# Optimization experiments

Measured on AMD Instinct MI355X. Metric: run time of the kernel, lower is better.

## Reference

```python
import jax, jax.numpy as jnp
import numpy as np

B, S, D_MODEL, H_DIM = 8, 4096, 512, 120  # h = 1, so d_k = h_dim = 120
NEG_INF = jnp.float32(-1e9)
L2_EPS = 1e-12  # F.normalize eps


def setup_inputs() -> dict:
    key = jax.random.key(0)
    k_q, k_m, k_w, k_wt = jax.random.split(key, 4)
    query = jax.random.normal(k_q, (B, S, D_MODEL), dtype=jnp.float32)
    mask = jax.random.randint(k_m, (B, S, S), 0, 2, dtype=jnp.int32)
    # q_linear params (kaiming-uniform-ish init scale)
    lim = 1.0 / np.sqrt(D_MODEL)
    w_q = jax.random.uniform(k_w, (H_DIM, D_MODEL), jnp.float32, -lim, lim)
    b_q = jnp.zeros((H_DIM,), jnp.float32)
    # weight_tensor: shape (h, d_k) = (1, 120), xavier-uniform scale
    wt_lim = np.sqrt(6.0 / (1 + H_DIM))
    weight_tensor = jax.random.uniform(k_wt, (1, H_DIM), jnp.float32, -wt_lim, wt_lim)
    return {"query": query, "mask": mask, "w_q": w_q, "b_q": b_q,
            "weight_tensor": weight_tensor}


def reference(query, mask, w_q, b_q, weight_tensor):
    # context = q_linear(query).view(B, -1, h_dim); with h=1 the view is identity
    context = jnp.einsum("bsd,kd->bsk", query, w_q) + b_q          # [B, S, 120]
    # weighted then L2-normalized (cosine-similarity) features
    ctx = context * weight_tensor[:, None, :]                        # bcast (1,1,120)
    norm = jnp.sqrt(jnp.sum(ctx * ctx, axis=-1, keepdims=True))
    ctx_n = ctx / jnp.maximum(norm, L2_EPS)
    scores = jnp.einsum("bqk,bpk->bqp", ctx_n, ctx_n)               # [B, S, S]
    scores = jnp.where(mask == 0, NEG_INF, scores)                   # masked_fill
    return jax.nn.softmax(scores, axis=-1)                           # dropout: eval/identity
```

## Files before the change

### kernel.cpp

```cpp
#include <hip/hip_runtime.h>
#include <hip/hip_bf16.h>
#include <stdint.h>

#define BATCH 8
#define SEQ   4096
#define DM    512
#define HD    120

typedef __bf16   v8bf  __attribute__((ext_vector_type(8)));
typedef float    v4f   __attribute__((ext_vector_type(4)));
typedef int      i4    __attribute__((ext_vector_type(4)));
typedef uint32_t u32x2 __attribute__((ext_vector_type(2)));
typedef uint32_t u32x4 __attribute__((ext_vector_type(4)));
typedef float    f32x4 __attribute__((ext_vector_type(4)));

static __device__ __forceinline__ ushort f2bf(float x) {
  uint32_t u = __builtin_bit_cast(uint32_t, x);
  return (ushort)((u + 0x7fffu + ((u >> 16) & 1u)) >> 16);
}

__global__ __launch_bounds__(256) void prep_kernel(
    const float* __restrict__ q, const float* __restrict__ wq,
    const float* __restrict__ bq, const float* __restrict__ wt,
    const int* __restrict__ mask, ushort* __restrict__ ctx,
    uint32_t* __restrict__ bits)
{
  __shared__ __align__(16) float qs[32][68];
  __shared__ __align__(16) float ws2[32][136];

  const int t = threadIdx.x;
  const int cb = blockIdx.x >> 1;

  if (blockIdx.x & 1) {
    const size_t row0 = (size_t)cb * 64;
    const int rhalf = t >> 7;
    const int pw    = t & 127;
    const int* mbase = mask + row0 * SEQ;
    uint32_t* bbase  = bits + row0 * 128;
    for (int s = 0; s < 32; ++s) {
      int row = s * 2 + rhalf;
      const int* mp = mbase + (size_t)row * SEQ + pw * 32;
      uint32_t wd = 0;
      #pragma unroll
      for (int k = 0; k < 8; ++k) {
        i4 m = *(const i4*)(mp + k * 4);
        wd |= (uint32_t)(m.x != 0) << (k * 4);
        wd |= (uint32_t)(m.y != 0) << (k * 4 + 1);
        wd |= (uint32_t)(m.z != 0) << (k * 4 + 2);
        wd |= (uint32_t)(m.w != 0) << (k * 4 + 3);
      }
      bbase[(size_t)row * 128 + pw] = wd;
    }
    return;
  }

  const int tx = t & 31, ty = t >> 5;
  const size_t row0 = (size_t)cb * 64;
  const int qr = t >> 2, qk = (t & 3) * 8;

  float acc[8][4];
  #pragma unroll
  for (int j = 0; j < 8; ++j)
    #pragma unroll
    for (int i = 0; i < 4; ++i) acc[j][i] = 0.f;

  for (int k0 = 0; k0 < DM; k0 += 32) {
    __syncthreads();
    {
      f32x4 v0 = *(const f32x4*)&q[(row0 + qr) * DM + k0 + qk];
      f32x4 v1 = *(const f32x4*)&q[(row0 + qr) * DM + k0 + qk + 4];
      #pragma unroll
      for (int i = 0; i < 4; ++i) qs[qk + i][qr] = v0[i];
      #pragma unroll
      for (int i = 0; i < 4; ++i) qs[qk + 4 + i][qr] = v1[i];
    }
    #pragma unroll
    for (int i = 0; i < 16; ++i) {
      int flat = t + i * 256;
      int kk = flat & 31, c = flat >> 5;
      ws2[kk][c] = (c < HD) ? wq[c * DM + k0 + kk] : 0.f;
    }
    __syncthreads();
    #pragma unroll
    for (int kk = 0; kk < 32; ++kk) {
      f32x4 bv = *(const f32x4*)&ws2[kk][tx * 4];
      f32x4 a0 = *(const f32x4*)&qs[kk][ty * 8];
      f32x4 a1 = *(const f32x4*)&qs[kk][ty * 8 + 4];
      #pragma unroll
      for (int r = 0; r < 4; ++r)
        #pragma unroll
        for (int c = 0; c < 4; ++c) {
          acc[r][c]     = fmaf(a0[r], bv[c], acc[r][c]);
          acc[4 + r][c] = fmaf(a1[r], bv[c], acc[4 + r][c]);
        }
    }
  }

  float wtv[4], bqv[4];
  #pragma unroll
  for (int i = 0; i < 4; ++i) {
    int c = tx * 4 + i;
    wtv[i] = (c < HD) ? wt[c] : 0.f;
    bqv[i] = (c < HD) ? bq[c] : 0.f;
  }
  #pragma unroll
  for (int j = 0; j < 8; ++j) {
    int r = ty * 8 + j;
    float v[4]; float ss = 0.f;
    #pragma unroll
    for (int i = 0; i < 4; ++i) {
      v[i] = (acc[j][i] + bqv[i]) * wtv[i];
      ss = fmaf(v[i], v[i], ss);
    }
    #pragma unroll
    for (int xm = 1; xm < 32; xm <<= 1) ss += __shfl_xor(ss, xm, 64);
    float rinv = 1.f / fmaxf(sqrtf(ss), 1e-12f);
    uint32_t p0 = (uint32_t)f2bf(v[0] * rinv) | ((uint32_t)f2bf(v[1] * rinv) << 16);
    uint32_t p1 = (uint32_t)f2bf(v[2] * rinv) | ((uint32_t)f2bf(v[3] * rinv) << 16);
    u32x2 o = {p0, p1};
    char* dst = (char*)ctx + (row0 + r) * 256 +
                (((tx >> 1) * 16) ^ ((r & 7) << 4)) + (tx & 1) * 8;
    *(u32x2*)dst = o;
  }
}

#define MFMA(A, B, C) __builtin_amdgcn_mfma_f32_16x16x32_bf16(A, B, C, 0, 0, 0)

static __device__ __forceinline__ v8bf ldfrag(const char* base, int row, int slot) {
  int byte = row * 256 + ((slot * 16) ^ ((row & 7) << 4));
  return __builtin_bit_cast(v8bf, *(const u32x4*)(base + byte));
}

#define STG_LOAD(R, j) do {                                                   \
  const char* _g = ctxb + (size_t)(j) * 16384 + w * 4096 + lane * 16;         \
  R##0 = *(const u32x4*)(_g);        R##1 = *(const u32x4*)(_g + 1024);       \
  R##2 = *(const u32x4*)(_g + 2048); R##3 = *(const u32x4*)(_g + 3072);       \
} while (0)

#define STG_WRITE(R, buf) do {                                                \
  char* _l = (buf) + w * 4096 + lane * 16;                                    \
  *(u32x4*)(_l)        = R##0;  *(u32x4*)(_l + 1024) = R##1;                  \
  *(u32x4*)(_l + 2048) = R##2;  *(u32x4*)(_l + 3072) = R##3;                  \
} while (0)

#define QKT(buf, acc) do {                                                    \
  _Pragma("unroll")                                                           \
  for (int _t = 0; _t < 4; ++_t) {                                            \
    acc[_t] = (v4f){0.f, 0.f, 0.f, 0.f};                                      \
    _Pragma("unroll")                                                         \
    for (int _k = 0; _k < 4; ++_k) {                                          \
      v8bf _a = ldfrag(buf, _t * 16 + ln, _k * 4 + g);                        \
      acc[_t] = MFMA(_a, qf[_k], acc[_t]);                                    \
    }                                                                         \
  }                                                                           \
} while (0)

#define EPIA(BW) do {                                                         \
  _Pragma("unroll")                                                           \
  for (int _t2 = 0; _t2 < 4; ++_t2) {                                         \
    uint32_t nib = ((_t2 < 2 ? (BW).x : (BW).y) >> ((_t2 & 1) * 16 + g * 4)); \
    _Pragma("unroll")                                                         \
    for (int _i = 0; _i < 4; ++_i) {                                          \
      float e = __expf(acc[_t2][_i] - 1.0f);                                  \
      lsum += ((nib >> _i) & 1u) ? e : 0.f;                                   \
    }                                                                         \
  }                                                                           \
} while (0)

#define EPIB(BW, j) do {                                                      \
  _Pragma("unroll")                                                           \
  for (int _t2 = 0; _t2 < 4; ++_t2) {                                         \
    uint32_t nib = ((_t2 < 2 ? (BW).x : (BW).y) >> ((_t2 & 1) * 16 + g * 4)); \
    f32x4 o;                                                                  \
    _Pragma("unroll")                                                         \
    for (int _i = 0; _i < 4; ++_i)                                            \
      o[_i] = ((nib >> _i) & 1u) ? __expf(acc[_t2][_i] - 1.0f) * lir : 0.f;   \
    *(f32x4*)(orow + (size_t)(j) * 64 + _t2 * 16 + g * 4) = o;                \
  }                                                                           \
} while (0)

#define BAR() do {                                                            \
  asm volatile("s_waitcnt lgkmcnt(0)" ::: "memory");                          \
  __builtin_amdgcn_s_barrier();                                               \
  __builtin_amdgcn_sched_barrier(0);                                          \
} while (0)

__global__ __launch_bounds__(256) void attn_kernel(
    const ushort* __restrict__ ctx, const uint32_t* __restrict__ bits,
    float* __restrict__ out)
{
  __shared__ __align__(16) char lds[32768];
  char* B0 = lds;
  char* B1 = lds + 16384;

  const int t    = threadIdx.x;
  const int b    = blockIdx.x & 7;
  const int tile = blockIdx.x >> 3;
  const int w    = t >> 6, lane = t & 63;
  const int ln   = lane & 15, g = lane >> 4;
  const int qrow = tile * 64 + w * 16 + ln;
  const char* ctxb = (const char*)ctx + (size_t)b * SEQ * 256;
  const uint32_t* __restrict__ brow = bits + ((size_t)b * SEQ + qrow) * 128;
  float*          __restrict__ orow = out + ((size_t)b * SEQ + qrow) * SEQ;

  v8bf qf[4];
  #pragma unroll
  for (int kk = 0; kk < 4; ++kk) {
    int slot = kk * 4 + g;
    qf[kk] = *(const v8bf*)(ctxb + (size_t)qrow * 256 +
                            ((slot * 16) ^ ((qrow & 7) << 4)));
  }

  u32x4 sA0, sA1, sA2, sA3, sB0, sB1, sB2, sB3;
  u32x2 bw0 = {0, 0}, bw1 = {0, 0}, bwn0 = {0, 0}, bwn1 = {0, 0};
  float lsum = 0.f;

  STG_LOAD(sA, 0);
  bw0 = *(const u32x2*)(brow);
  bw1 = *(const u32x2*)(brow + 2);
  STG_WRITE(sA, B0);
  STG_LOAD(sB, 1);
  __syncthreads();

  for (int jj = 0; jj < 64; jj += 2) {
    v4f acc[4];
    if (jj + 2 < 64) { STG_LOAD(sA, jj + 2); bwn0 = *(const u32x2*)(brow + (jj + 2) * 2); }
    QKT(B0, acc);
    STG_WRITE(sB, B1);
    EPIA(bw0);
    BAR();

    if (jj + 3 < 64) { STG_LOAD(sB, jj + 3); bwn1 = *(const u32x2*)(brow + (jj + 3) * 2); }
    QKT(B1, acc);
    if (jj + 2 < 64) STG_WRITE(sA, B0);
    EPIA(bw1);
    bw0 = bwn0; bw1 = bwn1;
    BAR();
  }

  lsum += __shfl_xor(lsum, 16, 64);
  lsum += __shfl_xor(lsum, 32, 64);
  const float lir = (lsum > 0.f) ? (1.f / lsum) : 0.f;

  STG_LOAD(sA, 0);
  bw0 = *(const u32x2*)(brow);
  bw1 = *(const u32x2*)(brow + 2);
  STG_WRITE(sA, B0);
  STG_LOAD(sB, 1);
  __syncthreads();

  for (int jj = 0; jj < 64; jj += 2) {
    v4f acc[4];
    if (jj + 2 < 64) { STG_LOAD(sA, jj + 2); bwn0 = *(const u32x2*)(brow + (jj + 2) * 2); }
    QKT(B0, acc);
    STG_WRITE(sB, B1);
    EPIB(bw0, jj);
    BAR();

    if (jj + 3 < 64) { STG_LOAD(sB, jj + 3); bwn1 = *(const u32x2*)(brow + (jj + 3) * 2); }
    QKT(B1, acc);
    if (jj + 2 < 64) STG_WRITE(sA, B0);
    EPIB(bw1, jj + 1);
    bw0 = bwn0; bw1 = bwn1;
    BAR();
  }
}

extern "C" void kernel_launch(void* const* d_in, const int* in_sizes, int n_in,
                              void* d_out, int out_size, void* d_ws, size_t ws_size,
                              hipStream_t stream) {
  const float* query = (const float*)d_in[0];
  const int*   mask  = (const int*)d_in[1];
  const float* w_q   = (const float*)d_in[2];
  const float* b_q   = (const float*)d_in[3];
  const float* wt    = (const float*)d_in[4];
  float* out = (float*)d_out;

  ushort*   ctx  = (ushort*)d_ws;
  uint32_t* bits = (uint32_t*)((char*)d_ws + (16u << 20));

  prep_kernel<<<dim3(1024), dim3(256), 0, stream>>>(query, w_q, b_q, wt, mask, ctx, bits);
  attn_kernel<<<dim3(512), dim3(256), 0, stream>>>(ctx, bits, out);
}
```

Baseline: 395.7 us.

## Switch attention to 32x32 MFMA with direct global fragment loads and key-split waves

Result: slower. 516.4 us (+30.5%).

```diff
diff --git a/kernel.cpp b/kernel.cpp
--- a/kernel.cpp
+++ b/kernel.cpp
@@ -8,7 +8,7 @@
 #define HD    120
 
 typedef __bf16   v8bf  __attribute__((ext_vector_type(8)));
-typedef float    v4f   __attribute__((ext_vector_type(4)));
+typedef float    v16f  __attribute__((ext_vector_type(16)));
 typedef int      i4    __attribute__((ext_vector_type(4)));
 typedef uint32_t u32x2 __attribute__((ext_vector_type(2)));
 typedef uint32_t u32x4 __attribute__((ext_vector_type(4)));
@@ -29,15 +29,15 @@
   __shared__ __align__(16) float ws2[32][136];
 
   const int t = threadIdx.x;
-  const int cb = blockIdx.x >> 1;
-
-  if (blockIdx.x & 1) {
-    const size_t row0 = (size_t)cb * 64;
+
+  if (blockIdx.x % 3 != 0) {
+    const int cb = blockIdx.x - blockIdx.x / 3 - 1;
+    const size_t row0 = (size_t)cb * 32;
     const int rhalf = t >> 7;
     const int pw    = t & 127;
     const int* mbase = mask + row0 * SEQ;
     uint32_t* bbase  = bits + row0 * 128;
-    for (int s = 0; s < 32; ++s) {
+    for (int s = 0; s < 16; ++s) {
       int row = s * 2 + rhalf;
       const int* mp = mbase + (size_t)row * SEQ + pw * 32;
       uint32_t wd = 0;
@@ -54,8 +54,9 @@
     return;
   }
 
+  const int gb = blockIdx.x / 3;
   const int tx = t & 31, ty = t >> 5;
-  const size_t row0 = (size_t)cb * 64;
+  const size_t row0 = (size_t)gb * 64;
   const int qr = t >> 2, qk = (t & 3) * 8;
 
   float acc[8][4];
@@ -118,151 +119,115 @@
     uint32_t p0 = (uint32_t)f2bf(v[0] * rinv) | ((uint32_t)f2bf(v[1] * rinv) << 16);
     uint32_t p1 = (uint32_t)f2bf(v[2] * rinv) | ((uint32_t)f2bf(v[3] * rinv) << 16);
     u32x2 o = {p0, p1};
-    char* dst = (char*)ctx + (row0 + r) * 256 +
-                (((tx >> 1) * 16) ^ ((r & 7) << 4)) + (tx & 1) * 8;
-    *(u32x2*)dst = o;
-  }
-}
-
-#define MFMA(A, B, C) __builtin_amdgcn_mfma_f32_16x16x32_bf16(A, B, C, 0, 0, 0)
-
-static __device__ __forceinline__ v8bf ldfrag(const char* base, int row, int slot) {
-  int byte = row * 256 + ((slot * 16) ^ ((row & 7) << 4));
-  return __builtin_bit_cast(v8bf, *(const u32x4*)(base + byte));
-}
-
-#define STG_LOAD(R, j) do {                                                   \
-  const char* _g = ctxb + (size_t)(j) * 16384 + w * 4096 + lane * 16;         \
-  R##0 = *(const u32x4*)(_g);        R##1 = *(const u32x4*)(_g + 1024);       \
-  R##2 = *(const u32x4*)(_g + 2048); R##3 = *(const u32x4*)(_g + 3072);       \
-} while (0)
-
-#define STG_WRITE(R, buf) do {                                                \
-  char* _l = (buf) + w * 4096 + lane * 16;                                    \
-  *(u32x4*)(_l)        = R##0;  *(u32x4*)(_l + 1024) = R##1;                  \
-  *(u32x4*)(_l + 2048) = R##2;  *(u32x4*)(_l + 3072) = R##3;                  \
-} while (0)
-
-#define QKT(buf, acc) do {                                                    \
+    *(u32x2*)((char*)ctx + (row0 + r) * 256 + tx * 8) = o;
+  }
+}
+
+#define MFMA32(A, B, C) __builtin_amdgcn_mfma_f32_32x32x16_bf16(A, B, C, 0, 0, 0)
+#define ZERO16 (v16f){0.f,0.f,0.f,0.f,0.f,0.f,0.f,0.f,0.f,0.f,0.f,0.f,0.f,0.f,0.f,0.f}
+
+#define LDA(R, tt) do {                                                       \
+  const char* _a = abase + (size_t)(tt) * 8192;                               \
+  R[0] = *(const v8bf*)(_a);        R[1] = *(const v8bf*)(_a + 32);           \
+  R[2] = *(const v8bf*)(_a + 64);   R[3] = *(const v8bf*)(_a + 96);           \
+  R[4] = *(const v8bf*)(_a + 128);  R[5] = *(const v8bf*)(_a + 160);          \
+  R[6] = *(const v8bf*)(_a + 192);  R[7] = *(const v8bf*)(_a + 224);          \
+} while (0)
+
+#define QKT32(R, acc) do {                                                    \
+  acc = ZERO16;                                                               \
+  acc = MFMA32(R[0], qf[0], acc);  acc = MFMA32(R[1], qf[1], acc);            \
+  acc = MFMA32(R[2], qf[2], acc);  acc = MFMA32(R[3], qf[3], acc);            \
+  acc = MFMA32(R[4], qf[4], acc);  acc = MFMA32(R[5], qf[5], acc);            \
+  acc = MFMA32(R[6], qf[6], acc);  acc = MFMA32(R[7], qf[7], acc);            \
+} while (0)
+
+#define STEPA(R, BW) do {                                                     \
+  v16f acc; QKT32(R, acc);                                                    \
   _Pragma("unroll")                                                           \
-  for (int _t = 0; _t < 4; ++_t) {                                            \
-    acc[_t] = (v4f){0.f, 0.f, 0.f, 0.f};                                      \
-    _Pragma("unroll")                                                         \
-    for (int _k = 0; _k < 4; ++_k) {                                          \
-      v8bf _a = ldfrag(buf, _t * 16 + ln, _k * 4 + g);                        \
-      acc[_t] = MFMA(_a, qf[_k], acc[_t]);                                    \
-    }                                                                         \
-  }                                                                           \
-} while (0)
-
-#define EPIA(BW) do {                                                         \
-  _Pragma("unroll")                                                           \
-  for (int _t2 = 0; _t2 < 4; ++_t2) {                                         \
-    uint32_t nib = ((_t2 < 2 ? (BW).x : (BW).y) >> ((_t2 & 1) * 16 + g * 4)); \
+  for (int _rq = 0; _rq < 4; ++_rq)                                           \
     _Pragma("unroll")                                                         \
     for (int _i = 0; _i < 4; ++_i) {                                          \
-      float e = __expf(acc[_t2][_i] - 1.0f);                                  \
-      lsum += ((nib >> _i) & 1u) ? e : 0.f;                                   \
+      float _e = __expf(acc[_rq * 4 + _i] - 1.0f);                            \
+      lsum += (((BW) >> (_rq * 8 + hi4 + _i)) & 1u) ? _e : 0.f;               \
     }                                                                         \
-  }                                                                           \
-} while (0)
-
-#define EPIB(BW, j) do {                                                      \
+} while (0)
+
+#define STEPB(R, BW, tt) do {                                                 \
+  v16f acc; QKT32(R, acc);                                                    \
   _Pragma("unroll")                                                           \
-  for (int _t2 = 0; _t2 < 4; ++_t2) {                                         \
-    uint32_t nib = ((_t2 < 2 ? (BW).x : (BW).y) >> ((_t2 & 1) * 16 + g * 4)); \
-    f32x4 o;                                                                  \
+  for (int _rq = 0; _rq < 4; ++_rq) {                                         \
+    f32x4 _o;                                                                 \
     _Pragma("unroll")                                                         \
     for (int _i = 0; _i < 4; ++_i)                                            \
-      o[_i] = ((nib >> _i) & 1u) ? __expf(acc[_t2][_i] - 1.0f) * lir : 0.f;   \
-    *(f32x4*)(orow + (size_t)(j) * 64 + _t2 * 16 + g * 4) = o;                \
+      _o[_i] = (((BW) >> (_rq * 8 + hi4 + _i)) & 1u)                          \
+                 ? __expf(acc[_rq * 4 + _i] - 1.0f) * lir : 0.f;              \
+    *(f32x4*)(orow + (tt) * 32 + _rq * 8) = _o;                               \
   }                                                                           \
-} while (0)
-
-#define BAR() do {                                                            \
-  asm volatile("s_waitcnt lgkmcnt(0)" ::: "memory");                          \
-  __builtin_amdgcn_s_barrier();                                               \
-  __builtin_amdgcn_sched_barrier(0);                                          \
 } while (0)
 
 __global__ __launch_bounds__(256) void attn_kernel(
     const ushort* __restrict__ ctx, const uint32_t* __restrict__ bits,
     float* __restrict__ out)
 {
-  __shared__ __align__(16) char lds[32768];
-  char* B0 = lds;
-  char* B1 = lds + 16384;
+  __shared__ float lW[128];
+  __shared__ float lfin[32];
 
   const int t    = threadIdx.x;
   const int b    = blockIdx.x & 7;
-  const int tile = blockIdx.x >> 3;
+  const int qg   = blockIdx.x >> 3;
   const int w    = t >> 6, lane = t & 63;
-  const int ln   = lane & 15, g = lane >> 4;
-  const int qrow = tile * 64 + w * 16 + ln;
+  const int q    = lane & 31, hi = lane >> 5;
+  const int hi4  = hi * 4;
+  const int q0   = qg * 32;
+  const int P0   = w * 1024;
+
   const char* ctxb = (const char*)ctx + (size_t)b * SEQ * 256;
-  const uint32_t* __restrict__ brow = bits + ((size_t)b * SEQ + qrow) * 128;
-  float*          __restrict__ orow = out + ((size_t)b * SEQ + qrow) * SEQ;
-
-  v8bf qf[4];
-  #pragma unroll
-  for (int kk = 0; kk < 4; ++kk) {
-    int slot = kk * 4 + g;
-    qf[kk] = *(const v8bf*)(ctxb + (size_t)qrow * 256 +
-                            ((slot * 16) ^ ((qrow & 7) << 4)));
-  }
-
-  u32x4 sA0, sA1, sA2, sA3, sB0, sB1, sB2, sB3;
-  u32x2 bw0 = {0, 0}, bw1 = {0, 0}, bwn0 = {0, 0}, bwn1 = {0, 0};
+  const char* abase = ctxb + (size_t)(P0 + q) * 256 + hi * 16;
+  const uint32_t* __restrict__ brow =
+      bits + ((size_t)b * SEQ + q0 + q) * 128 + (P0 >> 5);
+  float* __restrict__ orow =
+      out + ((size_t)b * SEQ + q0 + q) * SEQ + P0 + hi4;
+
+  const char* qp = ctxb + (size_t)(q0 + q) * 256 + hi * 16;
+  v8bf qf[8];
+  #pragma unroll
+  for (int kc = 0; kc < 8; ++kc) qf[kc] = *(const v8bf*)(qp + kc * 32);
+
+  v8bf SA[8], SB[8];
+  u32x4 BQc, BQn;
   float lsum = 0.f;
 
-  STG_LOAD(sA, 0);
-  bw0 = *(const u32x2*)(brow);
-  bw1 = *(const u32x2*)(brow + 2);
-  STG_WRITE(sA, B0);
-  STG_LOAD(sB, 1);
+  LDA(SA, 0); LDA(SB, 1);
+  BQc = *(const u32x4*)(brow);
+  for (int tt = 0; tt < 32; tt += 4) {
+    if (tt + 4 < 32) BQn = *(const u32x4*)(brow + tt + 4);
+    STEPA(SA, BQc[0]);  if (tt + 2 < 32) LDA(SA, tt + 2);
+    STEPA(SB, BQc[1]);  if (tt + 3 < 32) LDA(SB, tt + 3);
+    STEPA(SA, BQc[2]);  if (tt + 4 < 32) LDA(SA, tt + 4);
+    STEPA(SB, BQc[3]);  if (tt + 5 < 32) LDA(SB, tt + 5);
+    BQc = BQn;
+  }
+
+  lsum += __shfl_xor(lsum, 32, 64);
+  if (lane < 32) lW[w * 32 + lane] = lsum;
   __syncthreads();
-
-  for (int jj = 0; jj < 64; jj += 2) {
-    v4f acc[4];
-    if (jj + 2 < 64) { STG_LOAD(sA, jj + 2); bwn0 = *(const u32x2*)(brow + (jj + 2) * 2); }
-    QKT(B0, acc);
-    STG_WRITE(sB, B1);
-    EPIA(bw0);
-    BAR();
-
-    if (jj + 3 < 64) { STG_LOAD(sB, jj + 3); bwn1 = *(const u32x2*)(brow + (jj + 3) * 2); }
-    QKT(B1, acc);
-    if (jj + 2 < 64) STG_WRITE(sA, B0);
-    EPIA(bw1);
-    bw0 = bwn0; bw1 = bwn1;
-    BAR();
-  }
-
-  lsum += __shfl_xor(lsum, 16, 64);
-  lsum += __shfl_xor(lsum, 32, 64);
-  const float lir = (lsum > 0.f) ? (1.f / lsum) : 0.f;
-
-  STG_LOAD(sA, 0);
-  bw0 = *(const u32x2*)(brow);
-  bw1 = *(const u32x2*)(brow + 2);
-  STG_WRITE(sA, B0);
-  STG_LOAD(sB, 1);
+  if (t < 32) {
+    float lf = lW[t] + lW[32 + t] + lW[64 + t] + lW[96 + t];
+    lfin[t] = (lf > 0.f) ? (1.f / lf) : 0.f;
+  }
   __syncthreads();
-
-  for (int jj = 0; jj < 64; jj += 2) {
-    v4f acc[4];
-    if (jj + 2 < 64) { STG_LOAD(sA, jj + 2); bwn0 = *(const u32x2*)(brow + (jj + 2) * 2); }
-    QKT(B0, acc);
-    STG_WRITE(sB, B1);
-    EPIB(bw0, jj);
-    BAR();
-
-    if (jj + 3 < 64) { STG_LOAD(sB, jj + 3); bwn1 = *(const u32x2*)(brow + (jj + 3) * 2); }
-    QKT(B1, acc);
-    if (jj + 2 < 64) STG_WRITE(sA, B0);
-    EPIB(bw1, jj + 1);
-    bw0 = bwn0; bw1 = bwn1;
-    BAR();
+  const float lir = lfin[q];
+
+  LDA(SA, 0); LDA(SB, 1);
+  BQc = *(const u32x4*)(brow);
+  for (int tt = 0; tt < 32; tt += 4) {
+    if (tt + 4 < 32) BQn = *(const u32x4*)(brow + tt + 4);
+    STEPB(SA, BQc[0], tt);      if (tt + 2 < 32) LDA(SA, tt + 2);
+    STEPB(SB, BQc[1], tt + 1);  if (tt + 3 < 32) LDA(SB, tt + 3);
+    STEPB(SA, BQc[2], tt + 2);  if (tt + 4 < 32) LDA(SA, tt + 4);
+    STEPB(SB, BQc[3], tt + 3);  if (tt + 5 < 32) LDA(SB, tt + 5);
+    BQc = BQn;
   }
 }
 
@@ -279,6 +244,6 @@
   ushort*   ctx  = (ushort*)d_ws;
   uint32_t* bits = (uint32_t*)((char*)d_ws + (16u << 20));
 
-  prep_kernel<<<dim3(1024), dim3(256), 0, stream>>>(query, w_q, b_q, wt, mask, ctx, bits);
-  attn_kernel<<<dim3(512), dim3(256), 0, stream>>>(ctx, bits, out);
-}
+  prep_kernel<<<dim3(1536), dim3(256), 0, stream>>>(query, w_q, b_q, wt, mask, ctx, bits);
+  attn_kernel<<<dim3(1024), dim3(256), 0, stream>>>(ctx, bits, out);
+}
```

## Split attention into two key-half kernels with partial row sums and transposed mask bits

Applied to the files above, without the earlier changes.

After: 394.7 us (median of 2 runs). Within noise of the previous version (-0.3%).

```diff
diff --git a/kernel.cpp b/kernel.cpp
--- a/kernel.cpp
+++ b/kernel.cpp
@@ -6,6 +6,8 @@
 #define SEQ   4096
 #define DM    512
 #define HD    120
+#define PH    2048
+#define NT    32
 
 typedef __bf16   v8bf  __attribute__((ext_vector_type(8)));
 typedef float    v4f   __attribute__((ext_vector_type(4)));
@@ -23,23 +25,21 @@
     const float* __restrict__ q, const float* __restrict__ wq,
     const float* __restrict__ bq, const float* __restrict__ wt,
     const int* __restrict__ mask, ushort* __restrict__ ctx,
-    uint32_t* __restrict__ bits)
+    uint32_t* __restrict__ bitsT)
 {
-  __shared__ __align__(16) float qs[32][68];
-  __shared__ __align__(16) float ws2[32][136];
-
+  __shared__ __align__(16) char smem[33024];
   const int t = threadIdx.x;
-  const int cb = blockIdx.x >> 1;
 
   if (blockIdx.x & 1) {
+    uint32_t (*bw)[129] = (uint32_t(*)[129])smem;
+    const int cb = blockIdx.x >> 1;
     const size_t row0 = (size_t)cb * 64;
-    const int rhalf = t >> 7;
-    const int pw    = t & 127;
-    const int* mbase = mask + row0 * SEQ;
-    uint32_t* bbase  = bits + row0 * 128;
+    const int b     = (int)(row0 >> 12);
+    const int qbase = (int)(row0 & 4095);
+    const int rhalf = t >> 7, pw = t & 127;
     for (int s = 0; s < 32; ++s) {
       int row = s * 2 + rhalf;
-      const int* mp = mbase + (size_t)row * SEQ + pw * 32;
+      const int* mp = mask + (row0 + row) * SEQ + pw * 32;
       uint32_t wd = 0;
       #pragma unroll
       for (int k = 0; k < 8; ++k) {
@@ -49,13 +49,24 @@
         wd |= (uint32_t)(m.z != 0) << (k * 4 + 2);
         wd |= (uint32_t)(m.w != 0) << (k * 4 + 3);
       }
-      bbase[(size_t)row * 128 + pw] = wd;
+      bw[row][pw] = wd;
+    }
+    __syncthreads();
+    const int qq = t & 63, pg = t >> 6;
+    uint32_t* bT = bitsT + (size_t)b * 128 * 4096 + qbase + qq;
+    #pragma unroll 8
+    for (int i = 0; i < 32; ++i) {
+      int pw2 = pg * 32 + i;
+      bT[(size_t)pw2 * 4096] = bw[qq][pw2];
     }
     return;
   }
 
+  float (*qs)[68]   = (float(*)[68])smem;
+  float (*ws2)[136] = (float(*)[136])(smem + 8704);
+  const int gb = blockIdx.x >> 1;
   const int tx = t & 31, ty = t >> 5;
-  const size_t row0 = (size_t)cb * 64;
+  const size_t row0 = (size_t)gb * 64;
   const int qr = t >> 2, qk = (t & 3) * 8;
 
   float acc[8][4];
@@ -132,7 +143,7 @@
 }
 
 #define STG_LOAD(R, j) do {                                                   \
-  const char* _g = ctxb + (size_t)(j) * 16384 + w * 4096 + lane * 16;         \
+  const char* _g = ctxb + (size_t)(P0 + (j) * 64) * 256 + w * 4096 + lane * 16;\
   R##0 = *(const u32x4*)(_g);        R##1 = *(const u32x4*)(_g + 1024);       \
   R##2 = *(const u32x4*)(_g + 2048); R##3 = *(const u32x4*)(_g + 3072);       \
 } while (0)
@@ -155,10 +166,15 @@
   }                                                                           \
 } while (0)
 
-#define EPIA(BW) do {                                                         \
+#define LDB(x, y, tj) do {                                                    \
+  x = btb[(size_t)(tj) * 2 * 4096];                                           \
+  y = btb[((size_t)(tj) * 2 + 1) * 4096];                                     \
+} while (0)
+
+#define EPIA() do {                                                           \
   _Pragma("unroll")                                                           \
   for (int _t2 = 0; _t2 < 4; ++_t2) {                                         \
-    uint32_t nib = ((_t2 < 2 ? (BW).x : (BW).y) >> ((_t2 & 1) * 16 + g * 4)); \
+    uint32_t nib = ((_t2 < 2 ? bcx : bcy) >> ((_t2 & 1) * 16 + g * 4));       \
     _Pragma("unroll")                                                         \
     for (int _i = 0; _i < 4; ++_i) {                                          \
       float e = __expf(acc[_t2][_i] - 1.0f);                                  \
@@ -167,15 +183,15 @@
   }                                                                           \
 } while (0)
 
-#define EPIB(BW, j) do {                                                      \
+#define EPIB(tj) do {                                                         \
   _Pragma("unroll")                                                           \
   for (int _t2 = 0; _t2 < 4; ++_t2) {                                         \
-    uint32_t nib = ((_t2 < 2 ? (BW).x : (BW).y) >> ((_t2 & 1) * 16 + g * 4)); \
+    uint32_t nib = ((_t2 < 2 ? bcx : bcy) >> ((_t2 & 1) * 16 + g * 4));       \
     f32x4 o;                                                                  \
     _Pragma("unroll")                                                         \
     for (int _i = 0; _i < 4; ++_i)                                            \
       o[_i] = ((nib >> _i) & 1u) ? __expf(acc[_t2][_i] - 1.0f) * lir : 0.f;   \
-    *(f32x4*)(orow + (size_t)(j) * 64 + _t2 * 16 + g * 4) = o;                \
+    *(f32x4*)(orow + (size_t)(tj) * 64 + _t2 * 16 + g * 4) = o;               \
   }                                                                           \
 } while (0)
 
@@ -185,84 +201,94 @@
   __builtin_amdgcn_sched_barrier(0);                                          \
 } while (0)
 
-__global__ __launch_bounds__(256) void attn_kernel(
-    const ushort* __restrict__ ctx, const uint32_t* __restrict__ bits,
-    float* __restrict__ out)
+#define ATTN_COMMON                                                           \
+  __shared__ __align__(16) char lds[32768];                                   \
+  char* B0 = lds;                                                             \
+  char* B1 = lds + 16384;                                                     \
+  const int t    = threadIdx.x;                                               \
+  const int b    = blockIdx.x & 7;                                            \
+  const int rest = blockIdx.x >> 3;                                           \
+  const int ph   = rest & 1;                                                  \
+  const int qg   = rest >> 1;                                                 \
+  const int w    = t >> 6, lane = t & 63;                                     \
+  const int ln   = lane & 15, g = lane >> 4;                                  \
+  const int q0   = qg * 64;                                                   \
+  const int P0   = ph * PH;                                                   \
+  const int qrow = q0 + w * 16 + ln;                                          \
+  const char* ctxb = (const char*)ctx + (size_t)b * SEQ * 256;                \
+  const uint32_t* __restrict__ btb =                                          \
+      bitsT + ((size_t)b * 128 + (P0 >> 5)) * 4096 + qrow;                    \
+  v8bf qf[4];                                                                 \
+  _Pragma("unroll")                                                           \
+  for (int kk = 0; kk < 4; ++kk) {                                            \
+    int slot = kk * 4 + g;                                                    \
+    qf[kk] = *(const v8bf*)(ctxb + (size_t)qrow * 256 +                       \
+                            ((slot * 16) ^ ((qrow & 7) << 4)));               \
+  }                                                                           \
+  u32x4 sA0, sA1, sA2, sA3, sB0, sB1, sB2, sB3;                               \
+  uint32_t bcx, bcy, bnx = 0, bny = 0;
+
+__global__ __launch_bounds__(256) void attnA_kernel(
+    const ushort* __restrict__ ctx, const uint32_t* __restrict__ bitsT,
+    float* __restrict__ lpart)
 {
-  __shared__ __align__(16) char lds[32768];
-  char* B0 = lds;
-  char* B1 = lds + 16384;
-
-  const int t    = threadIdx.x;
-  const int b    = blockIdx.x & 7;
-  const int tile = blockIdx.x >> 3;
-  const int w    = t >> 6, lane = t & 63;
-  const int ln   = lane & 15, g = lane >> 4;
-  const int qrow = tile * 64 + w * 16 + ln;
-  const char* ctxb = (const char*)ctx + (size_t)b * SEQ * 256;
-  const uint32_t* __restrict__ brow = bits + ((size_t)b * SEQ + qrow) * 128;
-  float*          __restrict__ orow = out + ((size_t)b * SEQ + qrow) * SEQ;
-
-  v8bf qf[4];
-  #pragma unroll
-  for (int kk = 0; kk < 4; ++kk) {
-    int slot = kk * 4 + g;
-    qf[kk] = *(const v8bf*)(ctxb + (size_t)qrow * 256 +
-                            ((slot * 16) ^ ((qrow & 7) << 4)));
-  }
-
-  u32x4 sA0, sA1, sA2, sA3, sB0, sB1, sB2, sB3;
-  u32x2 bw0 = {0, 0}, bw1 = {0, 0}, bwn0 = {0, 0}, bwn1 = {0, 0};
+  ATTN_COMMON
   float lsum = 0.f;
 
   STG_LOAD(sA, 0);
-  bw0 = *(const u32x2*)(brow);
-  bw1 = *(const u32x2*)(brow + 2);
   STG_WRITE(sA, B0);
   STG_LOAD(sB, 1);
+  LDB(bcx, bcy, 0);
   __syncthreads();
 
-  for (int jj = 0; jj < 64; jj += 2) {
-    v4f acc[4];
-    if (jj + 2 < 64) { STG_LOAD(sA, jj + 2); bwn0 = *(const u32x2*)(brow + (jj + 2) * 2); }
-    QKT(B0, acc);
-    STG_WRITE(sB, B1);
-    EPIA(bw0);
+  for (int jj = 0; jj < NT; jj += 2) {
+    if (jj + 1 < NT) LDB(bnx, bny, jj + 1);
+    if (jj + 2 < NT) STG_LOAD(sA, jj + 2);
+    { v4f acc[4]; QKT(B0, acc); STG_WRITE(sB, B1); EPIA(); }
     BAR();
-
-    if (jj + 3 < 64) { STG_LOAD(sB, jj + 3); bwn1 = *(const u32x2*)(brow + (jj + 3) * 2); }
-    QKT(B1, acc);
-    if (jj + 2 < 64) STG_WRITE(sA, B0);
-    EPIA(bw1);
-    bw0 = bwn0; bw1 = bwn1;
+    bcx = bnx; bcy = bny;
+
+    if (jj + 2 < NT) LDB(bnx, bny, jj + 2);
+    if (jj + 3 < NT) STG_LOAD(sB, jj + 3);
+    { v4f acc[4]; QKT(B1, acc); if (jj + 2 < NT) STG_WRITE(sA, B0); EPIA(); }
     BAR();
+    bcx = bnx; bcy = bny;
   }
 
   lsum += __shfl_xor(lsum, 16, 64);
   lsum += __shfl_xor(lsum, 32, 64);
-  const float lir = (lsum > 0.f) ? (1.f / lsum) : 0.f;
+  if (g == 0)
+    lpart[(size_t)ph * (BATCH * SEQ) + (size_t)b * SEQ + qrow] = lsum;
+}
+
+__global__ __launch_bounds__(256) void attnB_kernel(
+    const ushort* __restrict__ ctx, const uint32_t* __restrict__ bitsT,
+    const float* __restrict__ lpart, float* __restrict__ out)
+{
+  ATTN_COMMON
+  const size_t grow = (size_t)b * SEQ + qrow;
+  const float lf = lpart[grow] + lpart[(size_t)(BATCH * SEQ) + grow];
+  const float lir = (lf > 0.f) ? (1.f / lf) : 0.f;
+  float* __restrict__ orow = out + grow * SEQ + P0;
 
   STG_LOAD(sA, 0);
-  bw0 = *(const u32x2*)(brow);
-  bw1 = *(const u32x2*)(brow + 2);
   STG_WRITE(sA, B0);
   STG_LOAD(sB, 1);
+  LDB(bcx, bcy, 0);
   __syncthreads();
 
-  for (int jj = 0; jj < 64; jj += 2) {
-    v4f acc[4];
-    if (jj + 2 < 64) { STG_LOAD(sA, jj + 2); bwn0 = *(const u32x2*)(brow + (jj + 2) * 2); }
-    QKT(B0, acc);
-    STG_WRITE(sB, B1);
-    EPIB(bw0, jj);
+  for (int jj = 0; jj < NT; jj += 2) {
+    if (jj + 1 < NT) LDB(bnx, bny, jj + 1);
+    if (jj + 2 < NT) STG_LOAD(sA, jj + 2);
+    { v4f acc[4]; QKT(B0, acc); STG_WRITE(sB, B1); EPIB(jj); }
     BAR();
-
-    if (jj + 3 < 64) { STG_LOAD(sB, jj + 3); bwn1 = *(const u32x2*)(brow + (jj + 3) * 2); }
-    QKT(B1, acc);
-    if (jj + 2 < 64) STG_WRITE(sA, B0);
-    EPIB(bw1, jj + 1);
-    bw0 = bwn0; bw1 = bwn1;
+    bcx = bnx; bcy = bny;
+
+    if (jj + 2 < NT) LDB(bnx, bny, jj + 2);
+    if (jj + 3 < NT) STG_LOAD(sB, jj + 3);
+    { v4f acc[4]; QKT(B1, acc); if (jj + 2 < NT) STG_WRITE(sA, B0); EPIB(jj + 1); }
     BAR();
+    bcx = bnx; bcy = bny;
   }
 }
 
@@ -276,9 +302,11 @@
   const float* wt    = (const float*)d_in[4];
   float* out = (float*)d_out;
 
-  ushort*   ctx  = (ushort*)d_ws;
-  uint32_t* bits = (uint32_t*)((char*)d_ws + (16u << 20));
-
-  prep_kernel<<<dim3(1024), dim3(256), 0, stream>>>(query, w_q, b_q, wt, mask, ctx, bits);
-  attn_kernel<<<dim3(512), dim3(256), 0, stream>>>(ctx, bits, out);
-}
+  ushort*   ctx   = (ushort*)d_ws;
+  uint32_t* bitsT = (uint32_t*)((char*)d_ws + (9u << 20));
+  float*    lpart = (float*)((char*)d_ws + (26u << 20));
+
+  prep_kernel <<<dim3(1024), dim3(256), 0, stream>>>(query, w_q, b_q, wt, mask, ctx, bitsT);
+  attnA_kernel<<<dim3(1024), dim3(256), 0, stream>>>(ctx, bitsT, lpart);
+  attnB_kernel<<<dim3(1024), dim3(256), 0, stream>>>(ctx, bitsT, lpart, out);
+}
```
